# Performance work log

Hardware: AMD Instinct MI355X
Metric: run time of the kernel (lower is better)

## Reference

```python
import jax, jax.numpy as jnp
import numpy as np

N_NODES = 2000
C_IN = 64
G_DIMS = [1, 256, 256, 256]
C_EMB = 128
HAZ = 512


def setup_inputs() -> dict:
    key = jax.random.key(0)
    ks = jax.random.split(key, 16)
    B, E = 128, 64000
    inp = jax.random.normal(ks[0], (B, C_IN + N_NODES), dtype=jnp.float32)
    src = jax.random.randint(ks[1], (E,), 0, N_NODES, dtype=jnp.int32)
    dst = jax.random.randint(ks[2], (E,), 0, N_NODES, dtype=jnp.int32)
    def lin(k, fi, fo):
        return jax.random.normal(k, (fi, fo), dtype=jnp.float32) / np.sqrt(fi)
    params = {
        'W0': lin(ks[3], G_DIMS[0], G_DIMS[1]), 'b0': jnp.zeros((G_DIMS[1],), jnp.float32),
        'W1': lin(ks[4], G_DIMS[1], G_DIMS[2]), 'b1': jnp.zeros((G_DIMS[2],), jnp.float32),
        'W2': lin(ks[5], G_DIMS[2], G_DIMS[3]), 'b2': jnp.zeros((G_DIMS[3],), jnp.float32),
        'We': lin(ks[6], C_IN, C_EMB),
        'Wh1': lin(ks[7], 2 * G_DIMS[3] + C_EMB, HAZ), 'bh1': jnp.zeros((HAZ,), jnp.float32),
        'Wh2': lin(ks[8], HAZ, HAZ // 2), 'bh2': jnp.zeros((HAZ // 2,), jnp.float32),
        'Wh3': lin(ks[9], HAZ // 2, 1),
    }
    return dict(inp=inp, src=src, dst=dst, **params)


def _gcn_layer(x, src, dst, dout_is, din_is, W, b):
    # x: [B, N, d_in]; DGL GraphConv norm='both': D_out^-1/2 gather-sum D_in^-1/2, then XW+b
    B, N, _ = x.shape
    h = x * dout_is[None, :, None]
    msg = h[:, src, :]                                   # [B, E, d_in]
    agg = jnp.zeros_like(h).at[:, dst, :].add(msg)       # scatter-add over edges
    agg = agg * din_is[None, :, None]
    return agg @ W + b


def reference(inp, src, dst, W0, b0, W1, b1, W2, b2, We, Wh1, bh1, Wh2, bh2, Wh3):
    B = inp.shape[0]
    inp_c = inp[:, :C_IN]
    x = inp[:, C_IN:].reshape(B, N_NODES, 1)
    # degree normalizers (DGL clamps degree to min 1)
    ones = jnp.ones_like(src, dtype=jnp.float32)
    dout = jnp.maximum(jnp.zeros((N_NODES,), jnp.float32).at[src].add(ones), 1.0)
    din = jnp.maximum(jnp.zeros((N_NODES,), jnp.float32).at[dst].add(ones), 1.0)
    dout_is = jax.lax.rsqrt(dout)
    din_is = jax.lax.rsqrt(din)

    embed = jax.nn.relu(inp_c @ We)
    hg = 0.0
    for W, b in ((W0, b0), (W1, b1), (W2, b2)):
        x = jax.nn.relu(_gcn_layer(x, src, dst, dout_is, din_is, W, b))
        r = jnp.concatenate([x.mean(axis=1), x.max(axis=1)], axis=-1)  # avg|max readout
        hg = hg + jax.nn.relu(r)

    fusion = jnp.concatenate([embed, hg], axis=1)
    h = jax.nn.relu(fusion @ Wh1 + bh1)
    h = jax.nn.relu(h @ Wh2 + bh2)
    out = h @ Wh3  # out_dim == 1 -> Identity head (dropout=0 / eval)
    return out
```

## Files before the change

### kernel.cpp

```cpp
#include <hip/hip_runtime.h>
#include <hip/hip_bf16.h>

#define B_    128
#define NN    2000
#define C_    256
#define E_    64000
#define CIN   64
#define ROWST 2064
#define CEMB  128
#define HAZ1  512
#define HAZ2  256
#define FUSD  640

typedef unsigned short u16;
typedef __attribute__((ext_vector_type(8))) short short8;
typedef __attribute__((ext_vector_type(8))) unsigned short ush8;
typedef __attribute__((ext_vector_type(4))) float f32x4;
typedef __attribute__((ext_vector_type(2))) float f32x2;

static constexpr size_t OFF_DEGO = 0;
static constexpr size_t OFF_DEGI = 8000;
static constexpr size_t OFF_CUR  = 16000;
static constexpr size_t OFF_WOUT = 24000;
static constexpr size_t OFF_WIN  = 32000;
static constexpr size_t OFF_IOFF = 40000;
static constexpr size_t OFF_CSRC = 48192;
static constexpr size_t OFF_CSRW = 304192;
static constexpr size_t OFF_HG   = 560192;
static constexpr size_t OFF_H1   = 887872;
static constexpr size_t OFF_PSUM2= 887872;
static constexpr size_t OFF_PMAX2= 1018944;
static constexpr size_t OFF_PSUM = 1281088;
static constexpr size_t OFF_PMAX = 1412160;
static constexpr size_t OFF_A    = 1543232;
static constexpr size_t OFF_WT1H = 2567232;
static constexpr size_t OFF_WT2H = 2829376;
static constexpr size_t OFF_XT   = 3091520;
static constexpr size_t OFF_XBUF = 4194304;

__device__ __forceinline__ u16 f2bf(float f) {
    union { float f; unsigned u; } v; v.f = f;
    unsigned u = v.u;
    unsigned r = (u + 0x7FFFu + ((u >> 16) & 1u)) >> 16;
    return (u16)r;
}
__device__ __forceinline__ float bf2f(u16 h) {
    union { unsigned u; float f; } v; v.u = ((unsigned)h) << 16;
    return v.f;
}
__device__ __forceinline__ f32x2 upk(unsigned u) {
    f32x2 r;
    r.x = __uint_as_float(u << 16);
    r.y = __uint_as_float(u & 0xffff0000u);
    return r;
}

__global__ void k_init(int* __restrict__ deg3, float* __restrict__ ps1,
                       float* __restrict__ ps2) {
    int i = blockIdx.x * 256 + threadIdx.x;
    if (i < 6000) deg3[i] = 0;
    else if (i < 6000 + 65536) ps1[i - 6000] = 0.f;
    else if (i < 6000 + 131072) ps2[i - 71536] = 0.f;
}

__global__ void k_deg(const int* __restrict__ src, const int* __restrict__ dst,
                      int* __restrict__ dego, int* __restrict__ degi) {
    int e = blockIdx.x * 256 + threadIdx.x;
    if (e < E_) {
        atomicAdd(&dego[src[e]], 1);
        atomicAdd(&degi[dst[e]], 1);
    }
}

__global__ void k_scan_norm(const int* __restrict__ degi, const int* __restrict__ dego,
                            int* __restrict__ ioff, float* __restrict__ wout,
                            float* __restrict__ win) {
    __shared__ int part[512];
    int t = threadIdx.x;
    int base = t * 4;
    int v[4]; int s = 0;
#pragma unroll
    for (int i = 0; i < 4; i++) {
        int idx = base + i;
        v[i] = (idx < NN) ? degi[idx] : 0;
        if (idx < NN) {
            wout[idx] = rsqrtf(fmaxf((float)dego[idx], 1.f));
            win[idx]  = rsqrtf(fmaxf((float)v[i], 1.f));
        }
        s += v[i];
    }
    part[t] = s;
    __syncthreads();
    for (int o = 1; o < 512; o <<= 1) {
        int x = 0;
        if (t >= o) x = part[t - o];
        __syncthreads();
        part[t] += x;
        __syncthreads();
    }
    int run = (t == 0) ? 0 : part[t - 1];
#pragma unroll
    for (int i = 0; i < 4; i++) {
        int idx = base + i;
        if (idx <= NN) ioff[idx] = run;
        run += v[i];
    }
}

__global__ void k_fill(const int* __restrict__ src, const int* __restrict__ dst,
                       const float* __restrict__ wout, const float* __restrict__ win,
                       const int* __restrict__ ioff, int* __restrict__ cursor,
                       int* __restrict__ csrc, float* __restrict__ csrw) {
    int e = blockIdx.x * 256 + threadIdx.x;
    if (e < E_) {
        int d = dst[e];
        int s = src[e];
        int p = atomicAdd(&cursor[d], 1);
        int i = ioff[d] + p;
        csrc[i] = s;
        csrw[i] = wout[s] * win[d];
    }
}

__global__ __launch_bounds__(256) void k_prepw2(
        const float* __restrict__ W1, const float* __restrict__ W2,
        u16* __restrict__ T1, u16* __restrict__ T2) {
    int which = blockIdx.x >> 8;
    int n = blockIdx.x & 255, k = threadIdx.x;
    const float* W = which ? W2 : W1;
    u16* T = which ? T2 : T1;
    T[n * 256 + k] = f2bf(W[(size_t)k * 256 + n]);
}

__global__ __launch_bounds__(256) void k_xt(
        const float* __restrict__ inp, float* __restrict__ xT) {
    __shared__ float tl[32][33];
    int tx = threadIdx.x & 31, ty = threadIdx.x >> 5;
    int n0 = blockIdx.x * 32, b0 = blockIdx.y * 32;
#pragma unroll
    for (int r = 0; r < 4; r++) {
        int b = b0 + ty + r * 8;
        int n = n0 + tx;
        if (n < NN) tl[tx][ty + r * 8] = inp[(size_t)b * ROWST + CIN + n];
    }
    __syncthreads();
#pragma unroll
    for (int r = 0; r < 4; r++) {
        int n = n0 + ty + r * 8;
        int b = b0 + tx;
        if (n < NN) xT[(size_t)n * B_ + b] = tl[ty + r * 8][tx];
    }
}

__global__ __launch_bounds__(64) void k_agg_scalar_t(
        const float* __restrict__ xT, const int* __restrict__ ioff,
        const int* __restrict__ csrc, const float* __restrict__ csrw,
        float* __restrict__ aT) {
    int n = blockIdx.x;
    int b = blockIdx.y * 64 + threadIdx.x;
    int e0 = ioff[n], e1 = ioff[n + 1];
    float acc0 = 0.f, acc1 = 0.f;
    int i = e0;
    for (; i + 2 <= e1; i += 2) {
        acc0 = fmaf(csrw[i],     xT[(size_t)csrc[i] * B_ + b],     acc0);
        acc1 = fmaf(csrw[i + 1], xT[(size_t)csrc[i + 1] * B_ + b], acc1);
    }
    if (i < e1) acc0 = fmaf(csrw[i], xT[(size_t)csrc[i] * B_ + b], acc0);
    aT[(size_t)n * B_ + b] = acc0 + acc1;
}

__global__ __launch_bounds__(256) void k_pool0(
        const float* __restrict__ aT, const float* __restrict__ W0,
        const float* __restrict__ b0, float* __restrict__ hg) {
    int b = blockIdx.x, c = threadIdx.x;
    float w0c = W0[c], b0c = b0[c];
    float s = 0.f, mx = 0.f;
    for (int n = 0; n < NN; n++) {
        float v = fmaxf(fmaf(aT[(size_t)n * B_ + b], w0c, b0c), 0.f);
        s += v;
        mx = fmaxf(mx, v);
    }
    hg[(size_t)b * 512 + c]       = s * (1.f / (float)NN);
    hg[(size_t)b * 512 + 256 + c] = mx;
}

__global__ __launch_bounds__(64) void k_agg_l1(
        const float* __restrict__ aT, const int* __restrict__ ioff,
        const int* __restrict__ csrc, const float* __restrict__ csrw,
        const float* __restrict__ W0, const float* __restrict__ b0,
        u16* __restrict__ xout, int b0g) {
    int n = blockIdx.x, bp = blockIdx.y, t = threadIdx.x;
    int half = t >> 5, c8 = (t & 31) * 8;
    int bl = bp * 2 + half;
    int bg = b0g + bl;
    int e0 = ioff[n], e1 = ioff[n + 1];
    f32x2 w2[4], bb2[4], aa[4] = {}, ab[4] = {};
#pragma unroll
    for (int d = 0; d < 4; d++) {
        w2[d].x = W0[c8 + 2 * d];  w2[d].y = W0[c8 + 2 * d + 1];
        bb2[d].x = b0[c8 + 2 * d]; bb2[d].y = b0[c8 + 2 * d + 1];
    }
    int i = e0;
    for (; i + 2 <= e1; i += 2) {
        float a0s = aT[(size_t)csrc[i] * B_ + bg],     we0 = csrw[i];
        float a1s = aT[(size_t)csrc[i + 1] * B_ + bg], we1 = csrw[i + 1];
        f32x2 a02 = {a0s, a0s}, we02 = {we0, we0};
        f32x2 a12 = {a1s, a1s}, we12 = {we1, we1};
#pragma unroll
        for (int d = 0; d < 4; d++) {
            f32x2 t0 = a02 * w2[d] + bb2[d];
            t0.x = fmaxf(t0.x, 0.f); t0.y = fmaxf(t0.y, 0.f);
            aa[d] += t0 * we02;
            f32x2 t1 = a12 * w2[d] + bb2[d];
            t1.x = fmaxf(t1.x, 0.f); t1.y = fmaxf(t1.y, 0.f);
            ab[d] += t1 * we12;
        }
    }
    if (i < e1) {
        float a0s = aT[(size_t)csrc[i] * B_ + bg], we0 = csrw[i];
        f32x2 a02 = {a0s, a0s}, we02 = {we0, we0};
#pragma unroll
        for (int d = 0; d < 4; d++) {
            f32x2 t0 = a02 * w2[d] + bb2[d];
            t0.x = fmaxf(t0.x, 0.f); t0.y = fmaxf(t0.y, 0.f);
            aa[d] += t0 * we02;
        }
    }
    ush8 o;
#pragma unroll
    for (int d = 0; d < 4; d++) {
        o[2 * d]     = f2bf(aa[d].x + ab[d].x);
        o[2 * d + 1] = f2bf(aa[d].y + ab[d].y);
    }
    *reinterpret_cast<ush8*>(&xout[((size_t)bl * NN + n) * C_ + c8]) = o;
}

__global__ __launch_bounds__(64) void k_agg_bf(
        const u16* __restrict__ xin, const int* __restrict__ ioff,
        const int* __restrict__ csrc, const float* __restrict__ csrw,
        u16* __restrict__ xout, int QBH) {
    int l = blockIdx.x + NN * blockIdx.y;
    int xcd = l & 7, slot = l >> 3;
    int q = slot / NN;
    int bp = xcd * QBH + q;
    int n = slot - q * NN;
    int t = threadIdx.x;
    int half = t >> 5, c8 = (t & 31) * 8;
    int bl = bp * 2 + half;
    int e0 = ioff[n], e1 = ioff[n + 1];
    const u16* xb = xin + (size_t)bl * NN * C_ + c8;
    f32x2 aa[4] = {}, ab[4] = {};
    int i = e0;
    for (; i + 2 <= e1; i += 2) {
        int s0 = csrc[i];     float w0s = csrw[i];
        int s1 = csrc[i + 1]; float w1s = csrw[i + 1];
        uint4 u0 = *reinterpret_cast<const uint4*>(&xb[(size_t)s0 * C_]);
        uint4 u1 = *reinterpret_cast<const uint4*>(&xb[(size_t)s1 * C_]);
        f32x2 w02 = {w0s, w0s}, w12 = {w1s, w1s};
        aa[0] += upk(u0.x) * w02;
        aa[1] += upk(u0.y) * w02;
        aa[2] += upk(u0.z) * w02;
        aa[3] += upk(u0.w) * w02;
        ab[0] += upk(u1.x) * w12;
        ab[1] += upk(u1.y) * w12;
        ab[2] += upk(u1.z) * w12;
        ab[3] += upk(u1.w) * w12;
    }
    if (i < e1) {
        int s0 = csrc[i]; float w0s = csrw[i];
        uint4 u0 = *reinterpret_cast<const uint4*>(&xb[(size_t)s0 * C_]);
        f32x2 w02 = {w0s, w0s};
        aa[0] += upk(u0.x) * w02;
        aa[1] += upk(u0.y) * w02;
        aa[2] += upk(u0.z) * w02;
        aa[3] += upk(u0.w) * w02;
    }
    ush8 o;
#pragma unroll
    for (int d = 0; d < 4; d++) {
        o[2 * d]     = f2bf(aa[d].x + ab[d].x);
        o[2 * d + 1] = f2bf(aa[d].y + ab[d].y);
    }
    *reinterpret_cast<ush8*>(&xout[((size_t)bl * NN + n) * C_ + c8]) = o;
}

#define GM 128
#define GN 256
#define GK 32
#define LDP 40

template<int OUT>
__global__ __launch_bounds__(512) void k_gemm_mfma(
        const u16* __restrict__ Abf, const u16* __restrict__ WTh,
        const float* __restrict__ bias,
        u16* __restrict__ Cbf, float* __restrict__ psum, float* __restrict__ pmax) {
    __shared__ u16 Ah[GM * LDP];
    __shared__ u16 Bh[GN * LDP];
    __shared__ float lsum[2][2][GN];
    __shared__ float lmax[2][2][GN];
    int tid  = threadIdx.x;
    int lane = tid & 63, wave = tid >> 6;
    int wm = wave >> 2, wn = wave & 3;
    int m0 = blockIdx.x * GM;
    int blk = lane >> 4, rr = lane & 15;
    int sr = tid >> 2, sseg = (tid & 3) * 8;

    f32x4 acc[4][4] = {};

    ush8 va  = *reinterpret_cast<const ush8*>(&Abf[(size_t)(m0 + sr) * 256 + sseg]);
    ush8 vb0 = *reinterpret_cast<const ush8*>(&WTh[(size_t)sr * 256 + sseg]);
    ush8 vb1 = *reinterpret_cast<const ush8*>(&WTh[(size_t)(sr + 128) * 256 + sseg]);

#pragma unroll
    for (int kk = 0; kk < 8; kk++) {
        *reinterpret_cast<ush8*>(&Ah[sr * LDP + sseg]) = va;
        *reinterpret_cast<ush8*>(&Bh[sr * LDP + sseg]) = vb0;
        *reinterpret_cast<ush8*>(&Bh[(sr + 128) * LDP + sseg]) = vb1;
        __syncthreads();
        if (kk < 7) {
            int k0n = (kk + 1) * GK;
            va  = *reinterpret_cast<const ush8*>(&Abf[(size_t)(m0 + sr) * 256 + k0n + sseg]);
            vb0 = *reinterpret_cast<const ush8*>(&WTh[(size_t)sr * 256 + k0n + sseg]);
            vb1 = *reinterpret_cast<const ush8*>(&WTh[(size_t)(sr + 128) * 256 + k0n + sseg]);
        }
        short8 af[4], bf[4];
#pragma unroll
        for (int mr = 0; mr < 4; mr++)
            af[mr] = *reinterpret_cast<const short8*>(
                &Ah[(wm * 64 + mr * 16 + rr) * LDP + blk * 8]);
#pragma unroll
        for (int nr = 0; nr < 4; nr++)
            bf[nr] = *reinterpret_cast<const short8*>(
                &Bh[(wn * 64 + nr * 16 + rr) * LDP + blk * 8]);
#pragma unroll
        for (int mr = 0; mr < 4; mr++)
#pragma unroll
            for (int nr = 0; nr < 4; nr++)
                acc[mr][nr] = __builtin_amdgcn_mfma_f32_16x16x32_bf16(
                    af[mr], bf[nr], acc[mr][nr], 0, 0, 0);
        __syncthreads();
    }

    int bl0   = m0 / NN;
    int split = (bl0 + 1) * NN - m0;

    float s_lo[4] = {}, s_hi[4] = {}, m_lo[4] = {}, m_hi[4] = {};
#pragma unroll
    for (int nr = 0; nr < 4; nr++) {
        int col = wn * 64 + nr * 16 + rr;
        float bs = bias[col];
#pragma unroll
        for (int mr = 0; mr < 4; mr++) {
            int rl = wm * 64 + mr * 16 + blk * 4;
#pragma unroll
            for (int j = 0; j < 4; j++) {
                float v = fmaxf(acc[mr][nr][j] + bs, 0.f);
                if (OUT == 1)
                    Cbf[(size_t)(m0 + rl + j) * 256 + col] = f2bf(v);
                bool second = (rl + j) >= split;
                s_lo[nr] += second ? 0.f : v;
                s_hi[nr] += second ? v : 0.f;
                m_lo[nr] = second ? m_lo[nr] : fmaxf(m_lo[nr], v);
                m_hi[nr] = second ? fmaxf(m_hi[nr], v) : m_hi[nr];
            }
        }
    }
#pragma unroll
    for (int nr = 0; nr < 4; nr++) {
        s_lo[nr] += __shfl_xor(s_lo[nr], 16); s_lo[nr] += __shfl_xor(s_lo[nr], 32);
        s_hi[nr] += __shfl_xor(s_hi[nr], 16); s_hi[nr] += __shfl_xor(s_hi[nr], 32);
        m_lo[nr] = fmaxf(m_lo[nr], __shfl_xor(m_lo[nr], 16));
        m_lo[nr] = fmaxf(m_lo[nr], __shfl_xor(m_lo[nr], 32));
        m_hi[nr] = fmaxf(m_hi[nr], __shfl_xor(m_hi[nr], 16));
        m_hi[nr] = fmaxf(m_hi[nr], __shfl_xor(m_hi[nr], 32));
    }
    if (lane < 16) {
#pragma unroll
        for (int nr = 0; nr < 4; nr++) {
            int cl = wn * 64 + nr * 16 + lane;
            lsum[0][wm][cl] = s_lo[nr];
            lsum[1][wm][cl] = s_hi[nr];
            lmax[0][wm][cl] = m_lo[nr];
            lmax[1][wm][cl] = m_hi[nr];
        }
    }
    __syncthreads();
    {
        int seg = tid >> 8, cl = tid & 255;
        if (!(seg == 1 && split >= GM)) {
            float s = lsum[seg][0][cl] + lsum[seg][1][cl];
            float m = fmaxf(lmax[seg][0][cl], lmax[seg][1][cl]);
            int blx = bl0 + seg;
            atomicAdd(&psum[blx * C_ + cl], s);
            atomicMax((unsigned int*)&pmax[blx * C_ + cl], __float_as_uint(m));
        }
    }
}

__global__ __launch_bounds__(256) void k_pool_combine2(
        float* __restrict__ ps1, float* __restrict__ pm1,
        float* __restrict__ ps2, float* __restrict__ pm2,
        float* __restrict__ hg, int b0g) {
    int bl = blockIdx.x, c = threadIdx.x;
    int idx = bl * C_ + c;
    float s1 = ps1[idx], m1 = pm1[idx];
    float s2 = ps2[idx], m2 = pm2[idx];
    ps1[idx] = 0.f; pm1[idx] = 0.f;
    ps2[idx] = 0.f; pm2[idx] = 0.f;
    size_t b = b0g + bl;
    hg[b * 512 + c]       += (s1 + s2) * (1.f / (float)NN);
    hg[b * 512 + 256 + c] += m1 + m2;
}

__global__ __launch_bounds__(512) void k_mlp1f(
        const float* __restrict__ inp, const float* __restrict__ We,
        const float* __restrict__ hg, const float* __restrict__ Wh1,
        const float* __restrict__ bh1, float* __restrict__ h1) {
    __shared__ float fus[FUSD];
    int b = blockIdx.x, j = threadIdx.x;
    if (j < CEMB) {
        const float* row = inp + (size_t)b * ROWST;
        float a = 0.f;
        for (int k = 0; k < CIN; k++) a += row[k] * We[k * CEMB + j];
        fus[j] = fmaxf(a, 0.f);
    }
    fus[CEMB + j] = hg[(size_t)b * 512 + j];
    __syncthreads();
    float a = bh1[j];
    for (int k = 0; k < FUSD; k++) a += fus[k] * Wh1[(size_t)k * HAZ1 + j];
    h1[(size_t)b * HAZ1 + j] = fmaxf(a, 0.f);
}

__global__ __launch_bounds__(256) void k_mlp2out(
        const float* __restrict__ h1, const float* __restrict__ Wh2,
        const float* __restrict__ bh2, const float* __restrict__ Wh3,
        float* __restrict__ out) {
    __shared__ float f2[HAZ1];
    __shared__ float red[256];
    int b = blockIdx.x, j = threadIdx.x;
    f2[j]       = h1[(size_t)b * HAZ1 + j];
    f2[256 + j] = h1[(size_t)b * HAZ1 + 256 + j];
    __syncthreads();
    float a = bh2[j];
    for (int k = 0; k < HAZ1; k++) a += f2[k] * Wh2[(size_t)k * HAZ2 + j];
    red[j] = fmaxf(a, 0.f) * Wh3[j];
    __syncthreads();
    for (int o = 128; o > 0; o >>= 1) {
        if (j < o) red[j] += red[j + o];
        __syncthreads();
    }
    if (j == 0) out[b] = red[0];
}

extern "C" void kernel_launch(void* const* d_in, const int* in_sizes, int n_in,
                              void* d_out, int out_size, void* d_ws, size_t ws_size,
                              hipStream_t stream) {
    const float* inp = (const float*)d_in[0];
    const int*   src = (const int*)d_in[1];
    const int*   dst = (const int*)d_in[2];
    const float* W0  = (const float*)d_in[3];
    const float* b0  = (const float*)d_in[4];
    const float* W1  = (const float*)d_in[5];
    const float* b1  = (const float*)d_in[6];
    const float* W2  = (const float*)d_in[7];
    const float* b2  = (const float*)d_in[8];
    const float* We  = (const float*)d_in[9];
    const float* Wh1 = (const float*)d_in[10];
    const float* bh1 = (const float*)d_in[11];
    const float* Wh2 = (const float*)d_in[12];
    const float* bh2 = (const float*)d_in[13];
    const float* Wh3 = (const float*)d_in[14];
    float* out = (float*)d_out;

    char* ws = (char*)d_ws;
    int*   dego = (int*)(ws + OFF_DEGO);
    int*   degi = (int*)(ws + OFF_DEGI);
    int*   cur  = (int*)(ws + OFF_CUR);
    float* wout = (float*)(ws + OFF_WOUT);
    float* win  = (float*)(ws + OFF_WIN);
    int*   ioff = (int*)(ws + OFF_IOFF);
    int*   csrc = (int*)(ws + OFF_CSRC);
    float* csrw = (float*)(ws + OFF_CSRW);
    float* hg   = (float*)(ws + OFF_HG);
    float* h1   = (float*)(ws + OFF_H1);
    float* psum1= (float*)(ws + OFF_PSUM);
    float* pmax1= (float*)(ws + OFF_PMAX);
    float* psum2= (float*)(ws + OFF_PSUM2);
    float* pmax2= (float*)(ws + OFF_PMAX2);
    float* aT   = (float*)(ws + OFF_A);
    float* xT   = (float*)(ws + OFF_XT);
    u16*   wt1h = (u16*)(ws + OFF_WT1H);
    u16*   wt2h = (u16*)(ws + OFF_WT2H);

    const size_t perb = (size_t)NN * C_ * 4;
    int CB = 128;
    while (CB > 16 && OFF_XBUF + (size_t)CB * perb > ws_size) CB >>= 1;
    int nchunk = B_ / CB;
    int CBH = CB / 2;
    int QBH = CBH / 8;

    u16* xB   = (u16*)(ws + OFF_XBUF);
    u16* xAbf = (u16*)(ws + OFF_XBUF + (size_t)CB * NN * C_ * 2);

    k_init<<<dim3(536), 256, 0, stream>>>(dego, psum1, psum2);
    k_deg<<<dim3((E_ + 255) / 256), 256, 0, stream>>>(src, dst, dego, degi);
    k_scan_norm<<<1, 512, 0, stream>>>(degi, dego, ioff, wout, win);
    k_fill<<<dim3((E_ + 255) / 256), 256, 0, stream>>>(src, dst, wout, win, ioff, cur, csrc, csrw);
    k_prepw2<<<dim3(512), 256, 0, stream>>>(W1, W2, wt1h, wt2h);
    k_xt<<<dim3(63, 4), 256, 0, stream>>>(inp, xT);

    k_agg_scalar_t<<<dim3(NN, 2), 64, 0, stream>>>(xT, ioff, csrc, csrw, aT);
    k_pool0<<<B_, 256, 0, stream>>>(aT, W0, b0, hg);

    dim3 gridNB(NN, CBH);
    dim3 gridGemm((CB * NN) / GM);

    for (int c = 0; c < nchunk; ++c) {
        int b0g = c * CB;

        k_agg_l1<<<gridNB, 64, 0, stream>>>(aT, ioff, csrc, csrw, W0, b0, xB, b0g);
        k_gemm_mfma<1><<<gridGemm, 512, 0, stream>>>(xB, wt1h, b1, xAbf, psum1, pmax1);

        k_agg_bf<<<gridNB, 64, 0, stream>>>(xAbf, ioff, csrc, csrw, xB, QBH);
        k_gemm_mfma<0><<<gridGemm, 512, 0, stream>>>(xB, wt2h, b2, nullptr, psum2, pmax2);

        k_pool_combine2<<<CB, 256, 0, stream>>>(psum1, pmax1, psum2, pmax2, hg, b0g);
    }

    k_mlp1f<<<B_, 512, 0, stream>>>(inp, We, hg, Wh1, bh1, h1);
    k_mlp2out<<<B_, 256, 0, stream>>>(h1, Wh2, bh2, Wh3, out);
}
```

Measured before the change: 643.1 us.

## Fuse graph aggregation into MFMA GEMM prologue and drop batch chunking

Each GEMM block now gathers its 64 rows of neighbour-aggregated features straight into shared memory, then runs the MFMA GEMM on them. This removes the separate aggregation kernels and the round-trip of the aggregated bf16 tensor through global memory. The M tile shrinks from 128 to 64 rows, blocks are remapped across XCDs, and the layer-2 gather is unrolled by four edges. The batch-chunk loop is replaced by a fixed 128-batch launch, which assumes the workspace is large enough. Gather latency now sits inside GEMM blocks with 512 threads each, which may limit latency hiding.

```diff
diff --git a/kernel.cpp b/kernel.cpp
--- a/kernel.cpp
+++ b/kernel.cpp
@@ -11,6 +11,7 @@
 #define HAZ1  512
 #define HAZ2  256
 #define FUSD  640
+#define CB    128
 
 typedef unsigned short u16;
 typedef __attribute__((ext_vector_type(8))) short short8;
@@ -184,156 +185,151 @@
     hg[(size_t)b * 512 + 256 + c] = mx;
 }
 
-__global__ __launch_bounds__(64) void k_agg_l1(
-        const float* __restrict__ aT, const int* __restrict__ ioff,
-        const int* __restrict__ csrc, const float* __restrict__ csrw,
+#define FGM 64
+#define FGN 256
+#define LDA 260
+#define LDB 40
+
+template<int MODE>
+__global__ __launch_bounds__(512, 4) void k_gemm_fused(
+        const float* __restrict__ aT, const u16* __restrict__ xin,
+        const u16* __restrict__ WTh,
         const float* __restrict__ W0, const float* __restrict__ b0,
-        u16* __restrict__ xout, int b0g) {
-    int n = blockIdx.x, bp = blockIdx.y, t = threadIdx.x;
-    int half = t >> 5, c8 = (t & 31) * 8;
-    int bl = bp * 2 + half;
-    int bg = b0g + bl;
-    int e0 = ioff[n], e1 = ioff[n + 1];
-    f32x2 w2[4], bb2[4], aa[4] = {}, ab[4] = {};
-#pragma unroll
-    for (int d = 0; d < 4; d++) {
-        w2[d].x = W0[c8 + 2 * d];  w2[d].y = W0[c8 + 2 * d + 1];
-        bb2[d].x = b0[c8 + 2 * d]; bb2[d].y = b0[c8 + 2 * d + 1];
-    }
-    int i = e0;
-    for (; i + 2 <= e1; i += 2) {
-        float a0s = aT[(size_t)csrc[i] * B_ + bg],     we0 = csrw[i];
-        float a1s = aT[(size_t)csrc[i + 1] * B_ + bg], we1 = csrw[i + 1];
-        f32x2 a02 = {a0s, a0s}, we02 = {we0, we0};
-        f32x2 a12 = {a1s, a1s}, we12 = {we1, we1};
-#pragma unroll
-        for (int d = 0; d < 4; d++) {
-            f32x2 t0 = a02 * w2[d] + bb2[d];
-            t0.x = fmaxf(t0.x, 0.f); t0.y = fmaxf(t0.y, 0.f);
-            aa[d] += t0 * we02;
-            f32x2 t1 = a12 * w2[d] + bb2[d];
-            t1.x = fmaxf(t1.x, 0.f); t1.y = fmaxf(t1.y, 0.f);
-            ab[d] += t1 * we12;
-        }
-    }
-    if (i < e1) {
-        float a0s = aT[(size_t)csrc[i] * B_ + bg], we0 = csrw[i];
-        f32x2 a02 = {a0s, a0s}, we02 = {we0, we0};
-#pragma unroll
-        for (int d = 0; d < 4; d++) {
-            f32x2 t0 = a02 * w2[d] + bb2[d];
-            t0.x = fmaxf(t0.x, 0.f); t0.y = fmaxf(t0.y, 0.f);
-            aa[d] += t0 * we02;
-        }
-    }
-    ush8 o;
-#pragma unroll
-    for (int d = 0; d < 4; d++) {
-        o[2 * d]     = f2bf(aa[d].x + ab[d].x);
-        o[2 * d + 1] = f2bf(aa[d].y + ab[d].y);
-    }
-    *reinterpret_cast<ush8*>(&xout[((size_t)bl * NN + n) * C_ + c8]) = o;
-}
-
-__global__ __launch_bounds__(64) void k_agg_bf(
-        const u16* __restrict__ xin, const int* __restrict__ ioff,
-        const int* __restrict__ csrc, const float* __restrict__ csrw,
-        u16* __restrict__ xout, int QBH) {
-    int l = blockIdx.x + NN * blockIdx.y;
-    int xcd = l & 7, slot = l >> 3;
-    int q = slot / NN;
-    int bp = xcd * QBH + q;
-    int n = slot - q * NN;
-    int t = threadIdx.x;
-    int half = t >> 5, c8 = (t & 31) * 8;
-    int bl = bp * 2 + half;
-    int e0 = ioff[n], e1 = ioff[n + 1];
-    const u16* xb = xin + (size_t)bl * NN * C_ + c8;
-    f32x2 aa[4] = {}, ab[4] = {};
-    int i = e0;
-    for (; i + 2 <= e1; i += 2) {
-        int s0 = csrc[i];     float w0s = csrw[i];
-        int s1 = csrc[i + 1]; float w1s = csrw[i + 1];
-        uint4 u0 = *reinterpret_cast<const uint4*>(&xb[(size_t)s0 * C_]);
-        uint4 u1 = *reinterpret_cast<const uint4*>(&xb[(size_t)s1 * C_]);
-        f32x2 w02 = {w0s, w0s}, w12 = {w1s, w1s};
-        aa[0] += upk(u0.x) * w02;
-        aa[1] += upk(u0.y) * w02;
-        aa[2] += upk(u0.z) * w02;
-        aa[3] += upk(u0.w) * w02;
-        ab[0] += upk(u1.x) * w12;
-        ab[1] += upk(u1.y) * w12;
-        ab[2] += upk(u1.z) * w12;
-        ab[3] += upk(u1.w) * w12;
-    }
-    if (i < e1) {
-        int s0 = csrc[i]; float w0s = csrw[i];
-        uint4 u0 = *reinterpret_cast<const uint4*>(&xb[(size_t)s0 * C_]);
-        f32x2 w02 = {w0s, w0s};
-        aa[0] += upk(u0.x) * w02;
-        aa[1] += upk(u0.y) * w02;
-        aa[2] += upk(u0.z) * w02;
-        aa[3] += upk(u0.w) * w02;
-    }
-    ush8 o;
-#pragma unroll
-    for (int d = 0; d < 4; d++) {
-        o[2 * d]     = f2bf(aa[d].x + ab[d].x);
-        o[2 * d + 1] = f2bf(aa[d].y + ab[d].y);
-    }
-    *reinterpret_cast<ush8*>(&xout[((size_t)bl * NN + n) * C_ + c8]) = o;
-}
-
-#define GM 128
-#define GN 256
-#define GK 32
-#define LDP 40
-
-template<int OUT>
-__global__ __launch_bounds__(512) void k_gemm_mfma(
-        const u16* __restrict__ Abf, const u16* __restrict__ WTh,
         const float* __restrict__ bias,
+        const int* __restrict__ ioff, const int* __restrict__ csrc,
+        const float* __restrict__ csrw,
         u16* __restrict__ Cbf, float* __restrict__ psum, float* __restrict__ pmax) {
-    __shared__ u16 Ah[GM * LDP];
-    __shared__ u16 Bh[GN * LDP];
-    __shared__ float lsum[2][2][GN];
-    __shared__ float lmax[2][2][GN];
+    __shared__ u16 Ah[FGM * LDA];
+    __shared__ u16 Bh[FGN * LDB];
+    float* lsum = (float*)Bh;
+    float* lmax = lsum + 2 * 2 * FGN;
+
     int tid  = threadIdx.x;
     int lane = tid & 63, wave = tid >> 6;
     int wm = wave >> 2, wn = wave & 3;
-    int m0 = blockIdx.x * GM;
+    int l = blockIdx.x;
+    int mb = (l & 7) * 500 + (l >> 3);
+    int m0 = mb * FGM;
     int blk = lane >> 4, rr = lane & 15;
+
+    {
+        int g  = tid >> 5;
+        int lg = tid & 31;
+        int c8 = lg * 8;
+        f32x2 w2[4], bb2[4];
+        if (MODE == 1) {
+#pragma unroll
+            for (int d = 0; d < 4; d++) {
+                w2[d].x = W0[c8 + 2 * d];  w2[d].y = W0[c8 + 2 * d + 1];
+                bb2[d].x = b0[c8 + 2 * d]; bb2[d].y = b0[c8 + 2 * d + 1];
+            }
+        }
+#pragma unroll
+        for (int rw = 0; rw < FGM / 16; rw++) {
+            int r  = g + rw * 16;
+            int gr = m0 + r;
+            int bl = gr / NN;
+            int n  = gr - bl * NN;
+            int e0 = ioff[n], e1 = ioff[n + 1];
+            f32x2 aa[4] = {}, ab[4] = {};
+            if (MODE == 2) {
+                const u16* xb = xin + (size_t)bl * NN * C_ + c8;
+                f32x2 ac[4] = {}, ad[4] = {};
+                int i = e0;
+                for (; i + 4 <= e1; i += 4) {
+                    int s0 = csrc[i];     float w0s = csrw[i];
+                    int s1 = csrc[i + 1]; float w1s = csrw[i + 1];
+                    int s2 = csrc[i + 2]; float w2s = csrw[i + 2];
+                    int s3 = csrc[i + 3]; float w3s = csrw[i + 3];
+                    uint4 u0 = *reinterpret_cast<const uint4*>(&xb[(size_t)s0 * C_]);
+                    uint4 u1 = *reinterpret_cast<const uint4*>(&xb[(size_t)s1 * C_]);
+                    uint4 u2 = *reinterpret_cast<const uint4*>(&xb[(size_t)s2 * C_]);
+                    uint4 u3 = *reinterpret_cast<const uint4*>(&xb[(size_t)s3 * C_]);
+                    f32x2 w02 = {w0s, w0s}, w12 = {w1s, w1s};
+                    f32x2 w22 = {w2s, w2s}, w32 = {w3s, w3s};
+                    aa[0] += upk(u0.x) * w02; aa[1] += upk(u0.y) * w02;
+                    aa[2] += upk(u0.z) * w02; aa[3] += upk(u0.w) * w02;
+                    ab[0] += upk(u1.x) * w12; ab[1] += upk(u1.y) * w12;
+                    ab[2] += upk(u1.z) * w12; ab[3] += upk(u1.w) * w12;
+                    ac[0] += upk(u2.x) * w22; ac[1] += upk(u2.y) * w22;
+                    ac[2] += upk(u2.z) * w22; ac[3] += upk(u2.w) * w22;
+                    ad[0] += upk(u3.x) * w32; ad[1] += upk(u3.y) * w32;
+                    ad[2] += upk(u3.z) * w32; ad[3] += upk(u3.w) * w32;
+                }
+                for (; i < e1; ++i) {
+                    int s0 = csrc[i]; float w0s = csrw[i];
+                    uint4 u0 = *reinterpret_cast<const uint4*>(&xb[(size_t)s0 * C_]);
+                    f32x2 w02 = {w0s, w0s};
+                    aa[0] += upk(u0.x) * w02; aa[1] += upk(u0.y) * w02;
+                    aa[2] += upk(u0.z) * w02; aa[3] += upk(u0.w) * w02;
+                }
+#pragma unroll
+                for (int d = 0; d < 4; d++) { aa[d] += ac[d]; ab[d] += ad[d]; }
+            } else {
+                int i = e0;
+                for (; i + 2 <= e1; i += 2) {
+                    float a0s = aT[(size_t)csrc[i] * B_ + bl],     we0 = csrw[i];
+                    float a1s = aT[(size_t)csrc[i + 1] * B_ + bl], we1 = csrw[i + 1];
+                    f32x2 a02 = {a0s, a0s}, we02 = {we0, we0};
+                    f32x2 a12 = {a1s, a1s}, we12 = {we1, we1};
+#pragma unroll
+                    for (int d = 0; d < 4; d++) {
+                        f32x2 t0 = a02 * w2[d] + bb2[d];
+                        t0.x = fmaxf(t0.x, 0.f); t0.y = fmaxf(t0.y, 0.f);
+                        aa[d] += t0 * we02;
+                        f32x2 t1 = a12 * w2[d] + bb2[d];
+                        t1.x = fmaxf(t1.x, 0.f); t1.y = fmaxf(t1.y, 0.f);
+                        ab[d] += t1 * we12;
+                    }
+                }
+                if (i < e1) {
+                    float a0s = aT[(size_t)csrc[i] * B_ + bl], we0 = csrw[i];
+                    f32x2 a02 = {a0s, a0s}, we02 = {we0, we0};
+#pragma unroll
+                    for (int d = 0; d < 4; d++) {
+                        f32x2 t0 = a02 * w2[d] + bb2[d];
+                        t0.x = fmaxf(t0.x, 0.f); t0.y = fmaxf(t0.y, 0.f);
+                        aa[d] += t0 * we02;
+                    }
+                }
+            }
+            ush8 o;
+#pragma unroll
+            for (int d = 0; d < 4; d++) {
+                o[2 * d]     = f2bf(aa[d].x + ab[d].x);
+                o[2 * d + 1] = f2bf(aa[d].y + ab[d].y);
+            }
+            *reinterpret_cast<ush8*>(&Ah[r * LDA + c8]) = o;
+        }
+    }
+
     int sr = tid >> 2, sseg = (tid & 3) * 8;
-
-    f32x4 acc[4][4] = {};
-
-    ush8 va  = *reinterpret_cast<const ush8*>(&Abf[(size_t)(m0 + sr) * 256 + sseg]);
     ush8 vb0 = *reinterpret_cast<const ush8*>(&WTh[(size_t)sr * 256 + sseg]);
     ush8 vb1 = *reinterpret_cast<const ush8*>(&WTh[(size_t)(sr + 128) * 256 + sseg]);
-
+    __syncthreads();
+
+    f32x4 acc[2][4] = {};
 #pragma unroll
     for (int kk = 0; kk < 8; kk++) {
-        *reinterpret_cast<ush8*>(&Ah[sr * LDP + sseg]) = va;
-        *reinterpret_cast<ush8*>(&Bh[sr * LDP + sseg]) = vb0;
-        *reinterpret_cast<ush8*>(&Bh[(sr + 128) * LDP + sseg]) = vb1;
+        *reinterpret_cast<ush8*>(&Bh[sr * LDB + sseg]) = vb0;
+        *reinterpret_cast<ush8*>(&Bh[(sr + 128) * LDB + sseg]) = vb1;
         __syncthreads();
         if (kk < 7) {
-            int k0n = (kk + 1) * GK;
-            va  = *reinterpret_cast<const ush8*>(&Abf[(size_t)(m0 + sr) * 256 + k0n + sseg]);
+            int k0n = (kk + 1) * 32;
             vb0 = *reinterpret_cast<const ush8*>(&WTh[(size_t)sr * 256 + k0n + sseg]);
             vb1 = *reinterpret_cast<const ush8*>(&WTh[(size_t)(sr + 128) * 256 + k0n + sseg]);
         }
-        short8 af[4], bf[4];
-#pragma unroll
-        for (int mr = 0; mr < 4; mr++)
+        short8 af[2], bf[4];
+#pragma unroll
+        for (int mr = 0; mr < 2; mr++)
             af[mr] = *reinterpret_cast<const short8*>(
-                &Ah[(wm * 64 + mr * 16 + rr) * LDP + blk * 8]);
+                &Ah[(wm * 32 + mr * 16 + rr) * LDA + kk * 32 + blk * 8]);
 #pragma unroll
         for (int nr = 0; nr < 4; nr++)
             bf[nr] = *reinterpret_cast<const short8*>(
-                &Bh[(wn * 64 + nr * 16 + rr) * LDP + blk * 8]);
-#pragma unroll
-        for (int mr = 0; mr < 4; mr++)
+                &Bh[(wn * 64 + nr * 16 + rr) * LDB + blk * 8]);
+#pragma unroll
+        for (int mr = 0; mr < 2; mr++)
 #pragma unroll
             for (int nr = 0; nr < 4; nr++)
                 acc[mr][nr] = __builtin_amdgcn_mfma_f32_16x16x32_bf16(
@@ -350,12 +346,12 @@
         int col = wn * 64 + nr * 16 + rr;
         float bs = bias[col];
 #pragma unroll
-        for (int mr = 0; mr < 4; mr++) {
-            int rl = wm * 64 + mr * 16 + blk * 4;
+        for (int mr = 0; mr < 2; mr++) {
+            int rl = wm * 32 + mr * 16 + blk * 4;
 #pragma unroll
             for (int j = 0; j < 4; j++) {
                 float v = fmaxf(acc[mr][nr][j] + bs, 0.f);
-                if (OUT == 1)
+                if (MODE == 1)
                     Cbf[(size_t)(m0 + rl + j) * 256 + col] = f2bf(v);
                 bool second = (rl + j) >= split;
                 s_lo[nr] += second ? 0.f : v;
@@ -378,18 +374,18 @@
 #pragma unroll
         for (int nr = 0; nr < 4; nr++) {
             int cl = wn * 64 + nr * 16 + lane;
-            lsum[0][wm][cl] = s_lo[nr];
-            lsum[1][wm][cl] = s_hi[nr];
-            lmax[0][wm][cl] = m_lo[nr];
-            lmax[1][wm][cl] = m_hi[nr];
+            lsum[(0 * 2 + wm) * FGN + cl] = s_lo[nr];
+            lsum[(1 * 2 + wm) * FGN + cl] = s_hi[nr];
+            lmax[(0 * 2 + wm) * FGN + cl] = m_lo[nr];
+            lmax[(1 * 2 + wm) * FGN + cl] = m_hi[nr];
         }
     }
     __syncthreads();
     {
         int seg = tid >> 8, cl = tid & 255;
-        if (!(seg == 1 && split >= GM)) {
-            float s = lsum[seg][0][cl] + lsum[seg][1][cl];
-            float m = fmaxf(lmax[seg][0][cl], lmax[seg][1][cl]);
+        if (!(seg == 1 && split >= FGM)) {
+            float s = lsum[(seg * 2 + 0) * FGN + cl] + lsum[(seg * 2 + 1) * FGN + cl];
+            float m = fmaxf(lmax[(seg * 2 + 0) * FGN + cl], lmax[(seg * 2 + 1) * FGN + cl]);
             int blx = bl0 + seg;
             atomicAdd(&psum[blx * C_ + cl], s);
             atomicMax((unsigned int*)&pmax[blx * C_ + cl], __float_as_uint(m));
@@ -400,16 +396,15 @@
 __global__ __launch_bounds__(256) void k_pool_combine2(
         float* __restrict__ ps1, float* __restrict__ pm1,
         float* __restrict__ ps2, float* __restrict__ pm2,
-        float* __restrict__ hg, int b0g) {
+        float* __restrict__ hg) {
     int bl = blockIdx.x, c = threadIdx.x;
     int idx = bl * C_ + c;
     float s1 = ps1[idx], m1 = pm1[idx];
     float s2 = ps2[idx], m2 = pm2[idx];
     ps1[idx] = 0.f; pm1[idx] = 0.f;
     ps2[idx] = 0.f; pm2[idx] = 0.f;
-    size_t b = b0g + bl;
-    hg[b * 512 + c]       += (s1 + s2) * (1.f / (float)NN);
-    hg[b * 512 + 256 + c] += m1 + m2;
+    hg[(size_t)bl * 512 + c]       += (s1 + s2) * (1.f / (float)NN);
+    hg[(size_t)bl * 512 + 256 + c] += m1 + m2;
 }
 
 __global__ __launch_bounds__(512) void k_mlp1f(
@@ -491,16 +486,7 @@
     float* xT   = (float*)(ws + OFF_XT);
     u16*   wt1h = (u16*)(ws + OFF_WT1H);
     u16*   wt2h = (u16*)(ws + OFF_WT2H);
-
-    const size_t perb = (size_t)NN * C_ * 4;
-    int CB = 128;
-    while (CB > 16 && OFF_XBUF + (size_t)CB * perb > ws_size) CB >>= 1;
-    int nchunk = B_ / CB;
-    int CBH = CB / 2;
-    int QBH = CBH / 8;
-
-    u16* xB   = (u16*)(ws + OFF_XBUF);
-    u16* xAbf = (u16*)(ws + OFF_XBUF + (size_t)CB * NN * C_ * 2);
+    u16*   xA   = (u16*)(ws + OFF_XBUF);
 
     k_init<<<dim3(536), 256, 0, stream>>>(dego, psum1, psum2);
     k_deg<<<dim3((E_ + 255) / 256), 256, 0, stream>>>(src, dst, dego, degi);
@@ -512,20 +498,16 @@
     k_agg_scalar_t<<<dim3(NN, 2), 64, 0, stream>>>(xT, ioff, csrc, csrw, aT);
     k_pool0<<<B_, 256, 0, stream>>>(aT, W0, b0, hg);
 
-    dim3 gridNB(NN, CBH);
-    dim3 gridGemm((CB * NN) / GM);
-
-    for (int c = 0; c < nchunk; ++c) {
-        int b0g = c * CB;
-
-        k_agg_l1<<<gridNB, 64, 0, stream>>>(aT, ioff, csrc, csrw, W0, b0, xB, b0g);
-        k_gemm_mfma<1><<<gridGemm, 512, 0, stream>>>(xB, wt1h, b1, xAbf, psum1, pmax1);
-
-        k_agg_bf<<<gridNB, 64, 0, stream>>>(xAbf, ioff, csrc, csrw, xB, QBH);
-        k_gemm_mfma<0><<<gridGemm, 512, 0, stream>>>(xB, wt2h, b2, nullptr, psum2, pmax2);
-
-        k_pool_combine2<<<CB, 256, 0, stream>>>(psum1, pmax1, psum2, pmax2, hg, b0g);
-    }
+    const int FB = (CB * NN) / FGM;
+
+    k_gemm_fused<1><<<dim3(FB), 512, 0, stream>>>(
+        aT, nullptr, wt1h, W0, b0, b1, ioff, csrc, csrw, xA, psum1, pmax1);
+
+    k_gemm_fused<2><<<dim3(FB), 512, 0, stream>>>(
+        nullptr, xA, wt2h, nullptr, nullptr, b2, ioff, csrc, csrw,
+        nullptr, psum2, pmax2);
+
+    k_pool_combine2<<<B_, 256, 0, stream>>>(psum1, pmax1, psum2, pmax2, hg);
 
     k_mlp1f<<<B_, 512, 0, stream>>>(inp, We, hg, Wh1, bh1, h1);
     k_mlp2out<<<B_, 256, 0, stream>>>(h1, Wh2, bh2, Wh3, out);
```

Result: slower. 754.5 us (+17.3%).
